# Performance work log

Hardware: AMD Instinct MI355X
Metric: run time of the kernel (lower is better)

Reference implementation:

```python
import jax, jax.numpy as jnp
import numpy as np

D_MODEL = 1024
N_HEADS = 16
D_HEAD = D_MODEL // N_HEADS
ROPE_BASE = 10000.0


def _rotate_half(x):
    half = x.shape[-1] // 2
    x1, x2 = x[..., :half], x[..., half:]
    return jnp.concatenate([-x2, x1], axis=-1)


def _rope_cos_sin(seq_len, d_head, dtype):
    inv_freq = 1.0 / (ROPE_BASE ** (jnp.arange(0, d_head, 2, dtype=jnp.float32) / d_head))
    t = jnp.arange(seq_len, dtype=jnp.float32)
    freqs = jnp.outer(t, inv_freq)                       # [S, d_head/2]
    emb = jnp.concatenate([freqs, freqs], axis=-1)       # [S, d_head]
    return jnp.cos(emb).astype(dtype), jnp.sin(emb).astype(dtype)


def setup_inputs() -> dict:
    key = jax.random.key(0)
    k1, k2, k3 = jax.random.split(key, 3)
    B, S = 2, 2048
    x = jax.random.normal(k1, (B, S, D_MODEL), dtype=jnp.float32)
    # torch nn.Linear weight layout: [out_features, in_features], y = x @ W.T
    w_qkv = jax.random.normal(k2, (3 * D_MODEL, D_MODEL), dtype=jnp.float32) * (D_MODEL ** -0.5)
    w_out = jax.random.normal(k3, (D_MODEL, D_MODEL), dtype=jnp.float32) * (D_MODEL ** -0.5)
    return {"x": x, "w_qkv": w_qkv, "w_out": w_out}


def reference(x, w_qkv, w_out):
    B, S, _ = x.shape
    qkv = jnp.einsum('bsd,ed->bse', x, w_qkv)            # [B, S, 3*D]
    qkv = qkv.reshape(B, S, 3, N_HEADS, D_HEAD)
    qkv = jnp.transpose(qkv, (2, 0, 3, 1, 4))            # [3, B, H, S, Dh]
    q, k, v = qkv[0], qkv[1], qkv[2]

    cos, sin = _rope_cos_sin(S, D_HEAD, x.dtype)         # [S, Dh] each
    cos = cos[None, None]                                # [1, 1, S, Dh]
    sin = sin[None, None]
    q = q * cos + _rotate_half(q) * sin
    k = k * cos + _rotate_half(k) * sin

    scale = 1.0 / jnp.sqrt(jnp.array(D_HEAD, dtype=x.dtype))
    attn = jnp.einsum('bhqd,bhkd->bhqk', q, k) * scale   # [B, H, S, S]
    causal = jnp.tril(jnp.ones((S, S), dtype=bool))      # triu(diag=1) masked -> keep lower tri
    attn = jnp.where(causal[None, None], attn, jnp.finfo(x.dtype).min)
    attn = jax.nn.softmax(attn, axis=-1)

    out = jnp.einsum('bhqk,bhkd->bhqd', attn, v)         # [B, H, S, Dh]
    out = jnp.transpose(out, (0, 2, 1, 3)).reshape(B, S, D_MODEL)
    return jnp.einsum('bsd,ed->bse', out, w_out)         # out_proj
```

## Files before the change

kernel.cpp:

```cpp
#include <hip/hip_runtime.h>
#include <hip/hip_bf16.h>
#include <cmath>

#define DMODEL 1024
#define NH 16
#define DH 64
#define SEQ 2048
#define BATCH 2

typedef __attribute__((ext_vector_type(8))) short bf16x8;
typedef __attribute__((ext_vector_type(4))) float f32x4;
typedef __attribute__((ext_vector_type(4))) unsigned int u32x4;
typedef __attribute__((ext_vector_type(8))) unsigned short u16x8;

typedef __attribute__((address_space(3))) unsigned int lds_u32;
typedef const __attribute__((address_space(1))) unsigned int g_u32;

__device__ __forceinline__ unsigned short f2bf(float f) {
    unsigned int u = __builtin_bit_cast(unsigned int, f);
    u += 0x7fffu + ((u >> 16) & 1u);
    return (unsigned short)(u >> 16);
}
__device__ __forceinline__ float exp2_fast(float x) {
    float r;
    asm("v_exp_f32 %0, %1" : "=v"(r) : "v"(x));
    return r;
}

__global__ __launch_bounds__(256)
void cast_all(const float* __restrict__ x, const float* __restrict__ wq,
              const float* __restrict__ wo, unsigned short* __restrict__ xb,
              unsigned short* __restrict__ wqb, unsigned short* __restrict__ wob)
{
    const int i = blockIdx.x * 256 + threadIdx.x;
    const float* src; unsigned short* dst; int off;
    if (i < 524288)      { src = x;  dst = xb;  off = i; }
    else if (i < 917504) { src = wq; dst = wqb; off = i - 524288; }
    else                 { src = wo; dst = wob; off = i - 917504; }
    const float4 a = *(const float4*)(src + (size_t)off * 8);
    const float4 b = *(const float4*)(src + (size_t)off * 8 + 4);
    u16x8 o;
    o[0] = f2bf(a.x); o[1] = f2bf(a.y); o[2] = f2bf(a.z); o[3] = f2bf(a.w);
    o[4] = f2bf(b.x); o[5] = f2bf(b.y); o[6] = f2bf(b.z); o[7] = f2bf(b.w);
    *(u16x8*)(dst + (size_t)off * 8) = o;
}

__global__ __launch_bounds__(512, 6)
void gemm_qkv(const unsigned short* __restrict__ A,
              const unsigned short* __restrict__ B,
              unsigned short* __restrict__ oq, unsigned short* __restrict__ ok,
              unsigned short* __restrict__ ovt)
{
    constexpr int K = 1024;
    constexpr int BK = 32;
    constexpr int NT = K / BK;
    __shared__ unsigned short As[2][128 * BK];
    __shared__ unsigned short Bs[2][128 * BK];

    const int t  = threadIdx.x;
    const int l  = t & 63;
    const int w  = t >> 6;
    const int g  = l >> 4;
    const int ln = l & 15;
    const int wr = w >> 2;
    const int wc = w & 3;
    const int m0 = blockIdx.y * 128;
    const int n0 = blockIdx.x * 128;
    const int cbase = (wc >> 1) * 64 + (wc & 1) * 16;

    auto stage = [&](int kt, int bufi) {
        const int r = t >> 2, slot = t & 3;
        const int kk = kt * BK + ((slot ^ ((r >> 1) & 3)) * 8);
        const unsigned short* ga = A + (size_t)(m0 + r) * K + kk;
        const unsigned short* gb = B + (size_t)(n0 + r) * K + kk;
        __builtin_amdgcn_global_load_lds((g_u32*)ga,
            (lds_u32*)&As[bufi][t * 8], 16, 0, 0);
        __builtin_amdgcn_global_load_lds((g_u32*)gb,
            (lds_u32*)&Bs[bufi][t * 8], 16, 0, 0);
    };

    f32x4 acc[4][2];
    #pragma unroll
    for (int i = 0; i < 4; ++i)
        #pragma unroll
        for (int j = 0; j < 2; ++j) acc[i][j] = (f32x4){0.f, 0.f, 0.f, 0.f};

    const int swz = (g ^ ((ln >> 1) & 3)) << 4;

    stage(0, 0);
    for (int kt = 0; kt < NT; ++kt) {
        __syncthreads();
        if (kt + 1 < NT) stage(kt + 1, (kt + 1) & 1);
        const char* as = (const char*)As[kt & 1];
        const char* bs = (const char*)Bs[kt & 1];
        bf16x8 af[4], bfr[2];
        #pragma unroll
        for (int fm = 0; fm < 4; ++fm)
            af[fm] = *(const bf16x8*)(as + (wr * 64 + fm * 16 + ln) * 64 + swz);
        #pragma unroll
        for (int fn = 0; fn < 2; ++fn)
            bfr[fn] = *(const bf16x8*)(bs + (cbase + fn * 32 + ln) * 64 + swz);
        #pragma unroll
        for (int fm = 0; fm < 4; ++fm)
            #pragma unroll
            for (int fn = 0; fn < 2; ++fn)
                acc[fm][fn] = __builtin_amdgcn_mfma_f32_16x16x32_bf16(
                    af[fm], bfr[fn], acc[fm][fn], 0, 0, 0);
    }

    const int rowbase = m0 + wr * 64;
    const int chead = n0 + (wc >> 1) * 64;
    const int which = chead >> 10;
    const int h = (chead >> 6) & (NH - 1);
    if (which < 2) {
        unsigned short* dst = which == 0 ? oq : ok;
        const float scale = which == 0 ? 0.18033688011112042f : 1.f;
        const float cexp = -13.287712379549449f / 32.f;
        const int d0 = (wc & 1) * 16 + ln;
        const float iff = exp2f((float)d0 * cexp);
        #pragma unroll
        for (int fm = 0; fm < 4; ++fm)
            #pragma unroll
            for (int rr = 0; rr < 4; ++rr) {
                const int row = rowbase + fm * 16 + g * 4 + rr;
                const int b = row >> 11, s = row & (SEQ - 1);
                float sn, cs;
                __sincosf((float)s * iff, &sn, &cs);
                const float x0 = acc[fm][0][rr], x1 = acc[fm][1][rr];
                const size_t base = (((size_t)b * NH + h) * SEQ + s) * DH;
                dst[base + d0]      = f2bf((x0 * cs - x1 * sn) * scale);
                dst[base + 32 + d0] = f2bf((x1 * cs + x0 * sn) * scale);
            }
    } else {
        #pragma unroll
        for (int fm = 0; fm < 4; ++fm)
            #pragma unroll
            for (int fn = 0; fn < 2; ++fn) {
                const int row = rowbase + fm * 16 + g * 4;
                const int b = row >> 11, s = row & (SEQ - 1);
                const int d = (wc & 1) * 16 + fn * 32 + ln;
                ushort4 pk;
                pk.x = f2bf(acc[fm][fn][0]); pk.y = f2bf(acc[fm][fn][1]);
                pk.z = f2bf(acc[fm][fn][2]); pk.w = f2bf(acc[fm][fn][3]);
                *(ushort4*)&ovt[(((size_t)b * NH + h) * DH + d) * SEQ + s] = pk;
            }
    }
}

__global__ __launch_bounds__(256)
void gemm_out(const unsigned short* __restrict__ A,
              const unsigned short* __restrict__ B,
              float* __restrict__ oc, int M, int N)
{
    constexpr int K = 1024;
    constexpr int BK = 32;
    constexpr int NT = K / BK;
    constexpr int BM = 64;
    constexpr int FM = 2;
    __shared__ unsigned short As[2][BM * BK];
    __shared__ unsigned short Bs[2][128 * BK];

    const int t  = threadIdx.x;
    const int l  = t & 63;
    const int w  = t >> 6;
    const int g  = l >> 4;
    const int ln = l & 15;
    const int wr = w >> 1, wc = w & 1;
    const int m0 = blockIdx.y * BM;
    const int n0 = blockIdx.x * 128;

    auto stage = [&](int kt, int bufi) {
        {
            const int r = t >> 2, slot = t & 3;
            const int kk = kt * BK + ((slot ^ ((r >> 1) & 3)) * 8);
            const unsigned short* ga = A + (size_t)(m0 + r) * K + kk;
            __builtin_amdgcn_global_load_lds((g_u32*)ga,
                (lds_u32*)&As[bufi][t * 8], 16, 0, 0);
        }
        #pragma unroll
        for (int i = 0; i < 2; ++i) {
            const int n = i * 256 + t;
            const int r = n >> 2, slot = n & 3;
            const int kk = kt * BK + ((slot ^ ((r >> 1) & 3)) * 8);
            const unsigned short* gb = B + (size_t)(n0 + r) * K + kk;
            __builtin_amdgcn_global_load_lds((g_u32*)gb,
                (lds_u32*)&Bs[bufi][n * 8], 16, 0, 0);
        }
    };

    f32x4 acc[FM][4];
    #pragma unroll
    for (int i = 0; i < FM; ++i)
        #pragma unroll
        for (int j = 0; j < 4; ++j) acc[i][j] = (f32x4){0.f, 0.f, 0.f, 0.f};

    const int swz = (g ^ ((ln >> 1) & 3)) << 4;

    stage(0, 0);
    for (int kt = 0; kt < NT; ++kt) {
        __syncthreads();
        if (kt + 1 < NT) stage(kt + 1, (kt + 1) & 1);
        const char* as = (const char*)As[kt & 1];
        const char* bs = (const char*)Bs[kt & 1];
        bf16x8 af[FM], bfr[4];
        #pragma unroll
        for (int fm = 0; fm < FM; ++fm)
            af[fm] = *(const bf16x8*)(as + (wr * (BM / 2) + fm * 16 + ln) * 64 + swz);
        #pragma unroll
        for (int fn = 0; fn < 4; ++fn)
            bfr[fn] = *(const bf16x8*)(bs + (wc * 64 + fn * 16 + ln) * 64 + swz);
        #pragma unroll
        for (int fm = 0; fm < FM; ++fm)
            #pragma unroll
            for (int fn = 0; fn < 4; ++fn)
                acc[fm][fn] = __builtin_amdgcn_mfma_f32_16x16x32_bf16(
                    af[fm], bfr[fn], acc[fm][fn], 0, 0, 0);
    }

    const int rowbase = m0 + wr * (BM / 2);
    const int colbase = n0 + wc * 64;
    #pragma unroll
    for (int fm = 0; fm < FM; ++fm)
        #pragma unroll
        for (int fn = 0; fn < 4; ++fn)
            #pragma unroll
            for (int rr = 0; rr < 4; ++rr) {
                const int row = rowbase + fm * 16 + g * 4 + rr;
                oc[(size_t)row * N + colbase + fn * 16 + ln] = acc[fm][fn][rr];
            }
}

__global__ __launch_bounds__(512, 4)
void attn_mfma(const unsigned short* __restrict__ q,
               const unsigned short* __restrict__ k,
               const unsigned short* __restrict__ vt,
               unsigned short* __restrict__ ob)
{
    __shared__ unsigned short Ks[2][64 * 64];
    __shared__ unsigned short Vs[2][64 * 64];

    const int t  = threadIdx.x;
    const int l  = t & 63;
    const int w  = t >> 6;
    const int wq = w & 3;
    const int g  = l >> 4;
    const int ln = l & 15;
    const int bid = blockIdx.x;
    const int xcd = bid & 7, jj = bid >> 3;
    const int bh = xcd * 4 + (jj >> 4);
    const int pi = jj & 15;
    const int qtA = pi, qtB = 31 - pi;
    const int myqt = (w < 4) ? qtA : qtB;
    const size_t bqk = (size_t)bh * SEQ * DH;
    const size_t bv  = (size_t)bh * DH * SEQ;

    bf16x8 qf0, qf1;
    {
        const unsigned short* qp = q + bqk + (size_t)(myqt * 64 + wq * 16 + ln) * DH + g * 8;
        qf0 = *(const bf16x8*)qp;
        qf1 = *(const bf16x8*)(qp + 32);
    }

    f32x4 ao[4];
    #pragma unroll
    for (int i = 0; i < 4; ++i) ao[i] = (f32x4){0.f, 0.f, 0.f, 0.f};
    float l_ = 0.f;

    auto stage = [&](int kt, int bufi) {
        const int row = t >> 3, sl = t & 7;
        const int sg  = (row & 3) | (((row >> 3) & 1) << 2);
        const int slg = (sl ^ sg) * 8;
        const unsigned short* gk = k  + bqk + (size_t)(kt * 64 + row) * DH + slg;
        const unsigned short* gv = vt + bv  + (size_t)row * SEQ + kt * 64 + slg;
        __builtin_amdgcn_global_load_lds((g_u32*)gk,
            (lds_u32*)&Ks[bufi][t * 8], 16, 0, 0);
        __builtin_amdgcn_global_load_lds((g_u32*)gv,
            (lds_u32*)&Vs[bufi][t * 8], 16, 0, 0);
    };

    const int rowoffK = ((ln >> 2) * 8 + (ln & 3)) * 128;
    const int sK = (ln & 3) | (((ln >> 2) & 1) << 2);
    const int slotK0 = ((g ^ sK) << 4);
    const int slotK1 = (((g + 4) ^ sK) << 4);
    const int sV = (ln & 3) | (((ln >> 3) & 1) << 2);

    stage(0, 0);
    for (int kt = 0; kt <= qtB; ++kt) {
        __syncthreads();
        if (kt < qtB) stage(kt + 1, (kt + 1) & 1);
        const bool act = (kt <= myqt);
        const char* kb = (const char*)Ks[kt & 1];
        const char* vb = (const char*)Vs[kt & 1];

        if (act) {
            f32x4 s[4];
            #pragma unroll
            for (int nb = 0; nb < 4; ++nb) s[nb] = (f32x4){0.f, 0.f, 0.f, 0.f};

            __builtin_amdgcn_s_setprio(1);
            #pragma unroll
            for (int nb = 0; nb < 4; ++nb) {
                const char* kr = kb + ((nb >> 1) * 32 + (nb & 1) * 4) * 128 + rowoffK;
                bf16x8 kf0 = *(const bf16x8*)(kr + slotK0);
                bf16x8 kf1 = *(const bf16x8*)(kr + slotK1);
                s[nb] = __builtin_amdgcn_mfma_f32_16x16x32_bf16(kf0, qf0, s[nb], 0, 0, 0);
                s[nb] = __builtin_amdgcn_mfma_f32_16x16x32_bf16(kf1, qf1, s[nb], 0, 0, 0);
            }
            __builtin_amdgcn_s_setprio(0);

            bf16x8 vf[8];
            #pragma unroll
            for (int ks = 0; ks < 2; ++ks)
                #pragma unroll
                for (int db = 0; db < 4; ++db) {
                    const int d = db * 16 + ln;
                    vf[ks * 4 + db] = *(const bf16x8*)(vb + d * 128 + (((ks * 4 + g) ^ sV) << 4));
                }

            if (kt == myqt) {
                #pragma unroll
                for (int nb = 0; nb < 4; ++nb)
                    #pragma unroll
                    for (int r = 0; r < 4; ++r)
                        if ((nb >> 1) * 32 + g * 8 + (nb & 1) * 4 + r > wq * 16 + ln)
                            s[nb][r] = -INFINITY;
            }

            const float M2 = 28.853900817779268f;
            bf16x8 pf[2];
            {
                float rs = 0.f;
                unsigned int dw[8];
                #pragma unroll
                for (int nb = 0; nb < 4; ++nb) {
                    float e[4];
                    #pragma unroll
                    for (int r = 0; r < 4; ++r)
                        e[r] = exp2_fast(s[nb][r] - M2);
                    rs += (e[0] + e[1]) + (e[2] + e[3]);
                    dw[nb * 2] = __builtin_amdgcn_perm(
                        __builtin_bit_cast(unsigned int, e[1]),
                        __builtin_bit_cast(unsigned int, e[0]), 0x07060302u);
                    dw[nb * 2 + 1] = __builtin_amdgcn_perm(
                        __builtin_bit_cast(unsigned int, e[3]),
                        __builtin_bit_cast(unsigned int, e[2]), 0x07060302u);
                }
                l_ += rs;
                pf[0] = __builtin_bit_cast(bf16x8, (u32x4){dw[0], dw[1], dw[2], dw[3]});
                pf[1] = __builtin_bit_cast(bf16x8, (u32x4){dw[4], dw[5], dw[6], dw[7]});
            }

            __builtin_amdgcn_s_setprio(1);
            #pragma unroll
            for (int ks = 0; ks < 2; ++ks)
                #pragma unroll
                for (int db = 0; db < 4; ++db)
                    ao[db] = __builtin_amdgcn_mfma_f32_16x16x32_bf16(
                        pf[ks], vf[ks * 4 + db], ao[db], 0, 0, 0);
            __builtin_amdgcn_s_setprio(0);
        }
    }

    l_ += __shfl_xor(l_, 16); l_ += __shfl_xor(l_, 32);
    const int b = bh >> 4, h = bh & (NH - 1);
    const float inv = 1.f / l_;
    #pragma unroll
    for (int r = 0; r < 4; ++r) {
        const float iv = __shfl(inv, g * 4 + r);
        const size_t row = (size_t)(b * SEQ + myqt * 64 + wq * 16 + g * 4 + r) * DMODEL + h * DH;
        #pragma unroll
        for (int db = 0; db < 4; ++db)
            ob[row + db * 16 + ln] = f2bf(ao[db][r] * iv);
    }
}

extern "C" void kernel_launch(void* const* d_in, const int* in_sizes, int n_in,
                              void* d_out, int out_size, void* d_ws, size_t ws_size,
                              hipStream_t stream)
{
    const float* x  = (const float*)d_in[0];
    const float* wq = (const float*)d_in[1];
    const float* wo = (const float*)d_in[2];
    float* out = (float*)d_out;

    const size_t NQ = (size_t)BATCH * NH * SEQ * DH;
    unsigned short* qb  = (unsigned short*)d_ws;
    unsigned short* kb  = qb + NQ;
    unsigned short* vtb = kb + NQ;
    unsigned short* ob  = vtb + NQ;
    unsigned short* xb  = ob + NQ;
    unsigned short* wqb = xb + NQ;
    unsigned short* wob = wqb + 3 * DMODEL * DMODEL;

    cast_all<<<4096, 256, 0, stream>>>(x, wq, wo, xb, wqb, wob);

    dim3 g1(3072 / 128, 4096 / 128);
    gemm_qkv<<<g1, 512, 0, stream>>>(xb, wqb, qb, kb, vtb);

    attn_mfma<<<512, 512, 0, stream>>>(qb, kb, vtb, ob);

    dim3 g3(1024 / 128, 4096 / 64);
    gemm_out<<<g3, 256, 0, stream>>>(ob, wob, out, 4096, 1024);
}
```

Baseline: 100.1 us.

## Process two KV tiles per barrier in attention; halve out-proj GEMM row tile

The attention kernel now keeps four K/V LDS buffers and handles two 64-key tiles per __syncthreads, prefetching the next pair while computing the current one. This halves the number of block barriers and gives loads more time to land. The output-projection GEMM tile shrinks from 64 to 32 rows, doubling the grid for better occupancy and load balance, at the cost of less B-tile reuse. The attention change doubles LDS use (64KB per block), which may lower occupancy.

After: 101.2 us. About the same (+1.1%).

```diff
diff --git a/kernel.cpp b/kernel.cpp
--- a/kernel.cpp
+++ b/kernel.cpp
@@ -155,8 +155,7 @@
     constexpr int K = 1024;
     constexpr int BK = 32;
     constexpr int NT = K / BK;
-    constexpr int BM = 64;
-    constexpr int FM = 2;
+    constexpr int BM = 32;
     __shared__ unsigned short As[2][BM * BK];
     __shared__ unsigned short Bs[2][128 * BK];
 
@@ -170,7 +169,7 @@
     const int n0 = blockIdx.x * 128;
 
     auto stage = [&](int kt, int bufi) {
-        {
+        if (t < 128) {
             const int r = t >> 2, slot = t & 3;
             const int kk = kt * BK + ((slot ^ ((r >> 1) & 3)) * 8);
             const unsigned short* ga = A + (size_t)(m0 + r) * K + kk;
@@ -188,11 +187,9 @@
         }
     };
 
-    f32x4 acc[FM][4];
+    f32x4 acc[4];
     #pragma unroll
-    for (int i = 0; i < FM; ++i)
-        #pragma unroll
-        for (int j = 0; j < 4; ++j) acc[i][j] = (f32x4){0.f, 0.f, 0.f, 0.f};
+    for (int j = 0; j < 4; ++j) acc[j] = (f32x4){0.f, 0.f, 0.f, 0.f};
 
     const int swz = (g ^ ((ln >> 1) & 3)) << 4;
 
@@ -202,32 +199,26 @@
         if (kt + 1 < NT) stage(kt + 1, (kt + 1) & 1);
         const char* as = (const char*)As[kt & 1];
         const char* bs = (const char*)Bs[kt & 1];
-        bf16x8 af[FM], bfr[4];
-        #pragma unroll
-        for (int fm = 0; fm < FM; ++fm)
-            af[fm] = *(const bf16x8*)(as + (wr * (BM / 2) + fm * 16 + ln) * 64 + swz);
+        bf16x8 af, bfr[4];
+        af = *(const bf16x8*)(as + (wr * 16 + ln) * 64 + swz);
         #pragma unroll
         for (int fn = 0; fn < 4; ++fn)
             bfr[fn] = *(const bf16x8*)(bs + (wc * 64 + fn * 16 + ln) * 64 + swz);
         #pragma unroll
-        for (int fm = 0; fm < FM; ++fm)
-            #pragma unroll
-            for (int fn = 0; fn < 4; ++fn)
-                acc[fm][fn] = __builtin_amdgcn_mfma_f32_16x16x32_bf16(
-                    af[fm], bfr[fn], acc[fm][fn], 0, 0, 0);
-    }
-
-    const int rowbase = m0 + wr * (BM / 2);
+        for (int fn = 0; fn < 4; ++fn)
+            acc[fn] = __builtin_amdgcn_mfma_f32_16x16x32_bf16(
+                af, bfr[fn], acc[fn], 0, 0, 0);
+    }
+
+    const int rowbase = m0 + wr * 16;
     const int colbase = n0 + wc * 64;
     #pragma unroll
-    for (int fm = 0; fm < FM; ++fm)
-        #pragma unroll
-        for (int fn = 0; fn < 4; ++fn)
-            #pragma unroll
-            for (int rr = 0; rr < 4; ++rr) {
-                const int row = rowbase + fm * 16 + g * 4 + rr;
-                oc[(size_t)row * N + colbase + fn * 16 + ln] = acc[fm][fn][rr];
-            }
+    for (int fn = 0; fn < 4; ++fn)
+        #pragma unroll
+        for (int rr = 0; rr < 4; ++rr) {
+            const int row = rowbase + g * 4 + rr;
+            oc[(size_t)row * N + colbase + fn * 16 + ln] = acc[fn][rr];
+        }
 }
 
 __global__ __launch_bounds__(512, 4)
@@ -236,8 +227,8 @@
                const unsigned short* __restrict__ vt,
                unsigned short* __restrict__ ob)
 {
-    __shared__ unsigned short Ks[2][64 * 64];
-    __shared__ unsigned short Vs[2][64 * 64];
+    __shared__ unsigned short Ks[4][64 * 64];
+    __shared__ unsigned short Vs[4][64 * 64];
 
     const int t  = threadIdx.x;
     const int l  = t & 63;
@@ -284,81 +275,88 @@
     const int slotK1 = (((g + 4) ^ sK) << 4);
     const int sV = (ln & 3) | (((ln >> 3) & 1) << 2);
 
+    auto compute = [&](int kt, int bufi) {
+        if (kt > myqt) return;
+        const char* kb = (const char*)Ks[bufi];
+        const char* vb = (const char*)Vs[bufi];
+
+        f32x4 s[4];
+        #pragma unroll
+        for (int nb = 0; nb < 4; ++nb) s[nb] = (f32x4){0.f, 0.f, 0.f, 0.f};
+
+        __builtin_amdgcn_s_setprio(1);
+        #pragma unroll
+        for (int nb = 0; nb < 4; ++nb) {
+            const char* kr = kb + ((nb >> 1) * 32 + (nb & 1) * 4) * 128 + rowoffK;
+            bf16x8 kf0 = *(const bf16x8*)(kr + slotK0);
+            bf16x8 kf1 = *(const bf16x8*)(kr + slotK1);
+            s[nb] = __builtin_amdgcn_mfma_f32_16x16x32_bf16(kf0, qf0, s[nb], 0, 0, 0);
+            s[nb] = __builtin_amdgcn_mfma_f32_16x16x32_bf16(kf1, qf1, s[nb], 0, 0, 0);
+        }
+        __builtin_amdgcn_s_setprio(0);
+
+        bf16x8 vf[8];
+        #pragma unroll
+        for (int ks = 0; ks < 2; ++ks)
+            #pragma unroll
+            for (int db = 0; db < 4; ++db) {
+                const int d = db * 16 + ln;
+                vf[ks * 4 + db] = *(const bf16x8*)(vb + d * 128 + (((ks * 4 + g) ^ sV) << 4));
+            }
+
+        if (kt == myqt) {
+            #pragma unroll
+            for (int nb = 0; nb < 4; ++nb)
+                #pragma unroll
+                for (int r = 0; r < 4; ++r)
+                    if ((nb >> 1) * 32 + g * 8 + (nb & 1) * 4 + r > wq * 16 + ln)
+                        s[nb][r] = -INFINITY;
+        }
+
+        const float M2 = 28.853900817779268f;
+        bf16x8 pf[2];
+        {
+            float rs = 0.f;
+            unsigned int dw[8];
+            #pragma unroll
+            for (int nb = 0; nb < 4; ++nb) {
+                float e[4];
+                #pragma unroll
+                for (int r = 0; r < 4; ++r)
+                    e[r] = exp2_fast(s[nb][r] - M2);
+                rs += (e[0] + e[1]) + (e[2] + e[3]);
+                dw[nb * 2] = __builtin_amdgcn_perm(
+                    __builtin_bit_cast(unsigned int, e[1]),
+                    __builtin_bit_cast(unsigned int, e[0]), 0x07060302u);
+                dw[nb * 2 + 1] = __builtin_amdgcn_perm(
+                    __builtin_bit_cast(unsigned int, e[3]),
+                    __builtin_bit_cast(unsigned int, e[2]), 0x07060302u);
+            }
+            l_ += rs;
+            pf[0] = __builtin_bit_cast(bf16x8, (u32x4){dw[0], dw[1], dw[2], dw[3]});
+            pf[1] = __builtin_bit_cast(bf16x8, (u32x4){dw[4], dw[5], dw[6], dw[7]});
+        }
+
+        __builtin_amdgcn_s_setprio(1);
+        #pragma unroll
+        for (int ks = 0; ks < 2; ++ks)
+            #pragma unroll
+            for (int db = 0; db < 4; ++db)
+                ao[db] = __builtin_amdgcn_mfma_f32_16x16x32_bf16(
+                    pf[ks], vf[ks * 4 + db], ao[db], 0, 0, 0);
+        __builtin_amdgcn_s_setprio(0);
+    };
+
     stage(0, 0);
-    for (int kt = 0; kt <= qtB; ++kt) {
+    if (qtB >= 1) stage(1, 1);
+    for (int kt = 0; kt <= qtB; kt += 2) {
+        const int bw = (kt >> 1) & 1;
         __syncthreads();
-        if (kt < qtB) stage(kt + 1, (kt + 1) & 1);
-        const bool act = (kt <= myqt);
-        const char* kb = (const char*)Ks[kt & 1];
-        const char* vb = (const char*)Vs[kt & 1];
-
-        if (act) {
-            f32x4 s[4];
-            #pragma unroll
-            for (int nb = 0; nb < 4; ++nb) s[nb] = (f32x4){0.f, 0.f, 0.f, 0.f};
-
-            __builtin_amdgcn_s_setprio(1);
-            #pragma unroll
-            for (int nb = 0; nb < 4; ++nb) {
-                const char* kr = kb + ((nb >> 1) * 32 + (nb & 1) * 4) * 128 + rowoffK;
-                bf16x8 kf0 = *(const bf16x8*)(kr + slotK0);
-                bf16x8 kf1 = *(const bf16x8*)(kr + slotK1);
-                s[nb] = __builtin_amdgcn_mfma_f32_16x16x32_bf16(kf0, qf0, s[nb], 0, 0, 0);
-                s[nb] = __builtin_amdgcn_mfma_f32_16x16x32_bf16(kf1, qf1, s[nb], 0, 0, 0);
-            }
-            __builtin_amdgcn_s_setprio(0);
-
-            bf16x8 vf[8];
-            #pragma unroll
-            for (int ks = 0; ks < 2; ++ks)
-                #pragma unroll
-                for (int db = 0; db < 4; ++db) {
-                    const int d = db * 16 + ln;
-                    vf[ks * 4 + db] = *(const bf16x8*)(vb + d * 128 + (((ks * 4 + g) ^ sV) << 4));
-                }
-
-            if (kt == myqt) {
-                #pragma unroll
-                for (int nb = 0; nb < 4; ++nb)
-                    #pragma unroll
-                    for (int r = 0; r < 4; ++r)
-                        if ((nb >> 1) * 32 + g * 8 + (nb & 1) * 4 + r > wq * 16 + ln)
-                            s[nb][r] = -INFINITY;
-            }
-
-            const float M2 = 28.853900817779268f;
-            bf16x8 pf[2];
-            {
-                float rs = 0.f;
-                unsigned int dw[8];
-                #pragma unroll
-                for (int nb = 0; nb < 4; ++nb) {
-                    float e[4];
-                    #pragma unroll
-                    for (int r = 0; r < 4; ++r)
-                        e[r] = exp2_fast(s[nb][r] - M2);
-                    rs += (e[0] + e[1]) + (e[2] + e[3]);
-                    dw[nb * 2] = __builtin_amdgcn_perm(
-                        __builtin_bit_cast(unsigned int, e[1]),
-                        __builtin_bit_cast(unsigned int, e[0]), 0x07060302u);
-                    dw[nb * 2 + 1] = __builtin_amdgcn_perm(
-                        __builtin_bit_cast(unsigned int, e[3]),
-                        __builtin_bit_cast(unsigned int, e[2]), 0x07060302u);
-                }
-                l_ += rs;
-                pf[0] = __builtin_bit_cast(bf16x8, (u32x4){dw[0], dw[1], dw[2], dw[3]});
-                pf[1] = __builtin_bit_cast(bf16x8, (u32x4){dw[4], dw[5], dw[6], dw[7]});
-            }
-
-            __builtin_amdgcn_s_setprio(1);
-            #pragma unroll
-            for (int ks = 0; ks < 2; ++ks)
-                #pragma unroll
-                for (int db = 0; db < 4; ++db)
-                    ao[db] = __builtin_amdgcn_mfma_f32_16x16x32_bf16(
-                        pf[ks], vf[ks * 4 + db], ao[db], 0, 0, 0);
-            __builtin_amdgcn_s_setprio(0);
-        }
+        const int nb2 = (bw ^ 1) * 2;
+        if (kt + 2 <= qtB) stage(kt + 2, nb2);
+        if (kt + 3 <= qtB) stage(kt + 3, nb2 + 1);
+        compute(kt, bw * 2);
+        if (kt + 1 <= qtB) compute(kt + 1, bw * 2 + 1);
     }
 
     l_ += __shfl_xor(l_, 16); l_ += __shfl_xor(l_, 32);
@@ -399,6 +397,6 @@
 
     attn_mfma<<<512, 512, 0, stream>>>(qb, kb, vtb, ob);
 
-    dim3 g3(1024 / 128, 4096 / 64);
+    dim3 g3(1024 / 128, 4096 / 32);
     gemm_out<<<g3, 256, 0, stream>>>(ob, wob, out, 4096, 1024);
 }
```

## Widen QKV GEMM tile to 128x256 so each wave owns a full head

Applied to the files above, without the earlier changes.

Doubles the N-dimension tile of the QKV projection GEMM from 128 to 256 columns. Each wave now computes a 64x64 sub-tile covering a whole head, so the RoPE epilogue pairs columns inside one wave. The change raises per-wave MFMA work relative to LDS A loads and halves the number of blocks reading A. In exchange it doubles the accumulator registers and the B shared-memory buffer, and lowers the occupancy hint from 6 to 4. The grid shrinks from 768 to 384 blocks, which may underfill the 256 CUs.

Result: slower. 102.7 us (+2.5%).

```diff
diff --git a/kernel.cpp b/kernel.cpp
--- a/kernel.cpp
+++ b/kernel.cpp
@@ -45,7 +45,7 @@
     *(u16x8*)(dst + (size_t)off * 8) = o;
 }
 
-__global__ __launch_bounds__(512, 6)
+__global__ __launch_bounds__(512, 4)
 void gemm_qkv(const unsigned short* __restrict__ A,
               const unsigned short* __restrict__ B,
               unsigned short* __restrict__ oq, unsigned short* __restrict__ ok,
@@ -55,7 +55,7 @@
     constexpr int BK = 32;
     constexpr int NT = K / BK;
     __shared__ unsigned short As[2][128 * BK];
-    __shared__ unsigned short Bs[2][128 * BK];
+    __shared__ unsigned short Bs[2][256 * BK];
 
     const int t  = threadIdx.x;
     const int l  = t & 63;
@@ -65,25 +65,32 @@
     const int wr = w >> 2;
     const int wc = w & 3;
     const int m0 = blockIdx.y * 128;
-    const int n0 = blockIdx.x * 128;
-    const int cbase = (wc >> 1) * 64 + (wc & 1) * 16;
+    const int n0 = blockIdx.x * 256;
 
     auto stage = [&](int kt, int bufi) {
-        const int r = t >> 2, slot = t & 3;
-        const int kk = kt * BK + ((slot ^ ((r >> 1) & 3)) * 8);
-        const unsigned short* ga = A + (size_t)(m0 + r) * K + kk;
-        const unsigned short* gb = B + (size_t)(n0 + r) * K + kk;
-        __builtin_amdgcn_global_load_lds((g_u32*)ga,
-            (lds_u32*)&As[bufi][t * 8], 16, 0, 0);
-        __builtin_amdgcn_global_load_lds((g_u32*)gb,
-            (lds_u32*)&Bs[bufi][t * 8], 16, 0, 0);
+        {
+            const int r = t >> 2, slot = t & 3;
+            const int kk = kt * BK + ((slot ^ ((r >> 1) & 3)) * 8);
+            const unsigned short* ga = A + (size_t)(m0 + r) * K + kk;
+            __builtin_amdgcn_global_load_lds((g_u32*)ga,
+                (lds_u32*)&As[bufi][t * 8], 16, 0, 0);
+        }
+        #pragma unroll
+        for (int i = 0; i < 2; ++i) {
+            const int n = i * 512 + t;
+            const int r = n >> 2, slot = n & 3;
+            const int kk = kt * BK + ((slot ^ ((r >> 1) & 3)) * 8);
+            const unsigned short* gb = B + (size_t)(n0 + r) * K + kk;
+            __builtin_amdgcn_global_load_lds((g_u32*)gb,
+                (lds_u32*)&Bs[bufi][n * 8], 16, 0, 0);
+        }
     };
 
-    f32x4 acc[4][2];
+    f32x4 acc[4][4];
     #pragma unroll
     for (int i = 0; i < 4; ++i)
         #pragma unroll
-        for (int j = 0; j < 2; ++j) acc[i][j] = (f32x4){0.f, 0.f, 0.f, 0.f};
+        for (int j = 0; j < 4; ++j) acc[i][j] = (f32x4){0.f, 0.f, 0.f, 0.f};
 
     const int swz = (g ^ ((ln >> 1) & 3)) << 4;
 
@@ -93,52 +100,56 @@
         if (kt + 1 < NT) stage(kt + 1, (kt + 1) & 1);
         const char* as = (const char*)As[kt & 1];
         const char* bs = (const char*)Bs[kt & 1];
-        bf16x8 af[4], bfr[2];
+        bf16x8 af[4], bfr[4];
         #pragma unroll
         for (int fm = 0; fm < 4; ++fm)
             af[fm] = *(const bf16x8*)(as + (wr * 64 + fm * 16 + ln) * 64 + swz);
         #pragma unroll
-        for (int fn = 0; fn < 2; ++fn)
-            bfr[fn] = *(const bf16x8*)(bs + (cbase + fn * 32 + ln) * 64 + swz);
+        for (int fn = 0; fn < 4; ++fn)
+            bfr[fn] = *(const bf16x8*)(bs + (wc * 64 + fn * 16 + ln) * 64 + swz);
         #pragma unroll
         for (int fm = 0; fm < 4; ++fm)
             #pragma unroll
-            for (int fn = 0; fn < 2; ++fn)
+            for (int fn = 0; fn < 4; ++fn)
                 acc[fm][fn] = __builtin_amdgcn_mfma_f32_16x16x32_bf16(
                     af[fm], bfr[fn], acc[fm][fn], 0, 0, 0);
     }
 
     const int rowbase = m0 + wr * 64;
-    const int chead = n0 + (wc >> 1) * 64;
+    const int chead = n0 + wc * 64;
     const int which = chead >> 10;
     const int h = (chead >> 6) & (NH - 1);
     if (which < 2) {
         unsigned short* dst = which == 0 ? oq : ok;
         const float scale = which == 0 ? 0.18033688011112042f : 1.f;
         const float cexp = -13.287712379549449f / 32.f;
-        const int d0 = (wc & 1) * 16 + ln;
-        const float iff = exp2f((float)d0 * cexp);
+        const float if0 = exp2f((float)ln * cexp);
+        const float if1 = exp2f((float)(16 + ln) * cexp);
         #pragma unroll
         for (int fm = 0; fm < 4; ++fm)
             #pragma unroll
             for (int rr = 0; rr < 4; ++rr) {
                 const int row = rowbase + fm * 16 + g * 4 + rr;
                 const int b = row >> 11, s = row & (SEQ - 1);
-                float sn, cs;
-                __sincosf((float)s * iff, &sn, &cs);
+                float s0, c0, s1, c1;
+                __sincosf((float)s * if0, &s0, &c0);
+                __sincosf((float)s * if1, &s1, &c1);
                 const float x0 = acc[fm][0][rr], x1 = acc[fm][1][rr];
+                const float x2 = acc[fm][2][rr], x3 = acc[fm][3][rr];
                 const size_t base = (((size_t)b * NH + h) * SEQ + s) * DH;
-                dst[base + d0]      = f2bf((x0 * cs - x1 * sn) * scale);
-                dst[base + 32 + d0] = f2bf((x1 * cs + x0 * sn) * scale);
+                dst[base + ln]      = f2bf((x0 * c0 - x2 * s0) * scale);
+                dst[base + 16 + ln] = f2bf((x1 * c1 - x3 * s1) * scale);
+                dst[base + 32 + ln] = f2bf((x2 * c0 + x0 * s0) * scale);
+                dst[base + 48 + ln] = f2bf((x3 * c1 + x1 * s1) * scale);
             }
     } else {
         #pragma unroll
         for (int fm = 0; fm < 4; ++fm)
             #pragma unroll
-            for (int fn = 0; fn < 2; ++fn) {
+            for (int fn = 0; fn < 4; ++fn) {
                 const int row = rowbase + fm * 16 + g * 4;
                 const int b = row >> 11, s = row & (SEQ - 1);
-                const int d = (wc & 1) * 16 + fn * 32 + ln;
+                const int d = fn * 16 + ln;
                 ushort4 pk;
                 pk.x = f2bf(acc[fm][fn][0]); pk.y = f2bf(acc[fm][fn][1]);
                 pk.z = f2bf(acc[fm][fn][2]); pk.w = f2bf(acc[fm][fn][3]);
@@ -394,7 +405,7 @@
 
     cast_all<<<4096, 256, 0, stream>>>(x, wq, wo, xb, wqb, wob);
 
-    dim3 g1(3072 / 128, 4096 / 128);
+    dim3 g1(3072 / 256, 4096 / 128);
     gemm_qkv<<<g1, 512, 0, stream>>>(xb, wqb, qb, kb, vtb);
 
     attn_mfma<<<512, 512, 0, stream>>>(qb, kb, vtb, ob);
```
